# Optimization experiments

Measured on AMD Instinct MI355X. Metric: run time of the kernel, lower is better.

Reference implementation:

```python
import jax, jax.numpy as jnp
from jax import lax
import numpy as np

KSIZE = 3      # matching patch size
RATE = 2       # down/up-sampling rate
STRIDE = 1
FUSE_K = 3     # diagonal fuse kernel (identity eye(3))
SCALE = 10.0   # softmax_scale


def same_pad(H, k, s):
    out = -(-H // s)
    pt = max((out - 1) * s + k - H, 0)
    return (pt // 2, pt - pt // 2)


def extract_patches(x, k, s):
    # x: [C,H,W] -> patches [L, C, k, k] with TF 'SAME' padding (matches torch extract_image_patches)
    C, H, W = x.shape
    ph = same_pad(H, k, s)
    pw = same_pad(W, k, s)
    xp = jnp.pad(x, ((0, 0), ph, pw))
    Hp, Wp = xp.shape[1], xp.shape[2]
    Ho = (Hp - k) // s + 1
    Wo = (Wp - k) // s + 1
    sl = [xp[:, i:i + (Ho - 1) * s + 1:s, j:j + (Wo - 1) * s + 1:s]
          for i in range(k) for j in range(k)]
    p = jnp.stack(sl, axis=1).reshape(C, k, k, Ho * Wo)  # [C,k,k,L]
    return p.transpose(3, 0, 1, 2)  # [L,C,k,k]


def diag_sum(t, k=FUSE_K):
    # conv2d with eye(k) kernel, SAME padding: out[p,q] = sum_d t[p+d-k//2, q+d-k//2]
    p0 = (k - 1) // 2
    p1 = k - 1 - p0
    tp = jnp.pad(t, ((p0, p1), (p0, p1)))
    H, W = t.shape
    return sum(tp[d:d + H, d:d + W] for d in range(k))


def attend_one(fi, bi):
    # fi, bi: [C,H,W] full resolution
    C, H, W = fi.shape
    kernel = 2 * RATE
    # patches for reconstruction, from full-res background
    raw_w = extract_patches(bi, kernel, RATE * STRIDE)  # [L,C,4,4]
    # nearest downsample by rate for matching
    fs = fi[:, ::RATE, ::RATE]
    bs = bi[:, ::RATE, ::RATE]
    Hs, Ws = fs.shape[1], fs.shape[2]
    L = Hs * Ws
    # matching patches from downscaled background, l2-normalized
    w = extract_patches(bs, KSIZE, STRIDE)  # [L,C,3,3]
    norm = jnp.sqrt(jnp.sum(w * w, axis=(1, 2, 3), keepdims=True))
    wn = (w / jnp.maximum(norm, 1e-4)).reshape(L, -1)  # [L, C*9]
    # correlation conv == im2col matmul: yi[l, q] = <patch_l(b), patch_q(f)>
    fp = extract_patches(fs, KSIZE, 1).reshape(L, -1)  # [HWf, C*9]
    yi = jnp.einsum('lp,qp->lq', wn, fp)  # [HWb, HWf]
    # fuse: propagate scores along diagonals in both orderings
    t = diag_sum(yi)
    t = t.reshape(Hs, Ws, Hs, Ws).transpose(1, 0, 3, 2).reshape(L, L)
    t = diag_sum(t)
    yi = t.reshape(Ws, Hs, Ws, Hs).transpose(1, 0, 3, 2).reshape(L, Hs, Ws)
    # softmax over background-patch axis
    att = jax.nn.softmax(yi * SCALE, axis=0)  # [L,Hs,Ws]
    # conv_transpose2d(att, raw_w, stride=2, padding=1) / 4  via overlap-add
    contrib = jnp.einsum('lhw,lcij->cijhw', att, raw_w)  # [C,4,4,Hs,Ws]
    buf = jnp.zeros((C, 2 * Hs + 2, 2 * Ws + 2), fi.dtype)
    for i in range(kernel):
        for j in range(kernel):
            buf = buf.at[:, i:i + 2 * Hs:2, j:j + 2 * Ws:2].add(contrib[:, i, j])
    return buf[:, 1:2 * Hs + 1, 1:2 * Ws + 1] / 4.0  # [C,H,W]


def conv3x3_elu(x, w, bias):
    y = lax.conv_general_dilated(x, w, (1, 1), [(1, 1), (1, 1)],
                                 dimension_numbers=('NCHW', 'OIHW', 'NCHW'))
    return jax.nn.elu(y + bias[None, :, None, None])


def setup_inputs() -> dict:
    key = jax.random.key(0)
    k1, k2, k3, k4 = jax.random.split(key, 4)
    B, C, H, W = 4, 128, 128, 128
    f = jax.random.normal(k1, (B, C, H, W), jnp.float32)
    b = jax.random.normal(k2, (B, C, H, W), jnp.float32)
    w1 = jax.random.normal(k3, (C, C, 3, 3), jnp.float32) * 0.02
    b1 = jnp.zeros((C,), jnp.float32)
    w2 = jax.random.normal(k4, (C, C, 3, 3), jnp.float32) * 0.02
    b2 = jnp.zeros((C,), jnp.float32)
    return {'f': f, 'b': b, 'w1': w1, 'b1': b1, 'w2': w2, 'b2': b2}


def reference(f, b, w1, b1, w2, b2):
    y = jax.vmap(attend_one)(f, b)  # [B,C,H,W]
    y = conv3x3_elu(y, w1, b1)
    y = conv3x3_elu(y, w2, b2)
    return y
```

## Files before the change

### kernel.cpp

```cpp
#include <hip/hip_runtime.h>
#include <math.h>

using u16 = unsigned short;
using u32 = unsigned int;
typedef _Float16 f16x8 __attribute__((ext_vector_type(8)));
typedef float    f32x4 __attribute__((ext_vector_type(4)));

union F16U { _Float16 h; u16 u; };
__device__ __forceinline__ u16 f2h(float f) { F16U x; x.h = (_Float16)f; return x.u; }
__device__ __forceinline__ float h2f(u16 v) { F16U x; x.u = v; return (float)x.h; }

__device__ __forceinline__ void gl16(const void* g, void* l) {
  __builtin_amdgcn_global_load_lds((const __attribute__((address_space(1))) void*)g,
                                   (__attribute__((address_space(3))) void*)l, 16, 0, 0);
}


__global__ void k_wperm(const float* __restrict__ w, u16* __restrict__ Wp) {
  int idx = blockIdx.x * 256 + threadIdx.x;
  if (idx < 147456) {
    int co = idx / 1152, r = idx - co * 1152, tap = r >> 7, ci = r & 127;
    Wp[idx] = f2h(w[((size_t)co * 128 + ci) * 9 + tap]);
  }
}

__global__ void k_extract(const float* __restrict__ fi, const float* __restrict__ bi,
                          u16* __restrict__ fh, u16* __restrict__ fl,
                          u16* __restrict__ bh, u16* __restrict__ bl) {
  __shared__ u16 lt[4][64][136];
  int ph = blockIdx.x, t = threadIdx.x;
  for (int it = 0; it < 32; ++it) {
    int idx = it * 256 + t;
    int c = idx >> 6, pw = idx & 63;
    int src = c * 16384 + (2 * ph) * 128 + 2 * pw;
    float vf = fi[src], vb = bi[src];
    u16 fhi = f2h(vf), flo = f2h(vf - h2f(fhi));
    u16 bhi = f2h(vb), blo = f2h(vb - h2f(bhi));
    lt[0][pw][c] = fhi; lt[1][pw][c] = flo; lt[2][pw][c] = bhi; lt[3][pw][c] = blo;
  }
  __syncthreads();
  for (int it = 0; it < 16; ++it) {
    int g = it * 256 + t;
    int arr = g >> 10, rem = g & 1023, pw = rem >> 4, slot = rem & 15;
    uint4 v = *(const uint4*)&lt[arr][pw][slot * 8];
    u16* o = (arr == 0) ? fh : (arr == 1) ? fl : (arr == 2) ? bh : bl;
    *(uint4*)&o[(size_t)(ph * 64 + pw) * 128 + slot * 8] = v;
  }
}

__global__ void k_norm(const u16* __restrict__ bh, const u16* __restrict__ bl,
                       float* __restrict__ nrm) {
  int wid = threadIdx.x >> 6, lane = threadIdx.x & 63;
  int l = blockIdx.x * 4 + wid;
  int lh = l >> 6, lw = l & 63;
  float s = 0.f;
#pragma unroll
  for (int dh = -1; dh <= 1; ++dh)
#pragma unroll
    for (int dw = -1; dw <= 1; ++dw) {
      int y = lh + dh, x = lw + dw;
      if ((u32)y < 64u && (u32)x < 64u) {
        int p = y * 64 + x;
        u32 h2 = *(const u32*)&bh[(size_t)p * 128 + lane * 2];
        u32 l2 = *(const u32*)&bl[(size_t)p * 128 + lane * 2];
        float v0 = h2f((u16)h2) + h2f((u16)l2);
        float v1 = h2f((u16)(h2 >> 16)) + h2f((u16)(l2 >> 16));
        s += v0 * v0 + v1 * v1;
      }
    }
#pragma unroll
  for (int off = 32; off; off >>= 1) s += __shfl_xor(s, off);
  if (lane == 0) nrm[l] = sqrtf(s);
}

__global__ __launch_bounds__(256) void k_rgemm(const u16* __restrict__ fh, const u16* __restrict__ fl,
                                               const u16* __restrict__ bh, const u16* __restrict__ bl,
                                               float* __restrict__ C) {
  __shared__ u16 lds[4 * 128 * 64];
  u16* Ah = lds; u16* Al = lds + 8192; u16* Bh = lds + 16384; u16* Bl = lds + 24576;
  int t = threadIdx.x, lane = t & 63, wid = t >> 6;
  int wm = (wid >> 1) * 64, wn = (wid & 1) * 64;
  int fr = lane & 15, kb = lane >> 4;
  int b = blockIdx.x;
  int xcd = b & 7, r = b >> 3;
  int by = xcd * 4 + (r & 3), bx = r >> 2;
  int q0 = by * 128, l0 = bx * 128;
  f32x4 acc[4][4] = {};
  for (int kt = 0; kt < 128; kt += 64) {
#pragma unroll
    for (int j = 0; j < 4; ++j) {
      int g = wid * 256 + j * 64 + lane;
      int row = g >> 3, s = (g & 7) ^ (row & 7);
      int co = kt + s * 8;
      size_t ldso = (size_t)(wid * 256 + j * 64) * 8;
      gl16(&fh[(size_t)(q0 + row) * 128 + co], Ah + ldso);
      gl16(&fl[(size_t)(q0 + row) * 128 + co], Al + ldso);
      gl16(&bh[(size_t)(l0 + row) * 128 + co], Bh + ldso);
      gl16(&bl[(size_t)(l0 + row) * 128 + co], Bl + ldso);
    }
    __syncthreads();
#pragma unroll
    for (int kf = 0; kf < 2; ++kf) {
      f16x8 ah[4], al4[4], bh4[4], bl4[4];
#pragma unroll
      for (int mi = 0; mi < 4; ++mi) {
        int row = wm + mi * 16 + fr;
        int off = row * 64 + ((kf * 4 + kb) ^ (row & 7)) * 8;
        ah[mi] = *(const f16x8*)&Ah[off];
        al4[mi] = *(const f16x8*)&Al[off];
      }
#pragma unroll
      for (int ni = 0; ni < 4; ++ni) {
        int row = wn + ni * 16 + fr;
        int off = row * 64 + ((kf * 4 + kb) ^ (row & 7)) * 8;
        bh4[ni] = *(const f16x8*)&Bh[off];
        bl4[ni] = *(const f16x8*)&Bl[off];
      }
#pragma unroll
      for (int mi = 0; mi < 4; ++mi)
#pragma unroll
        for (int ni = 0; ni < 4; ++ni) {
          acc[mi][ni] = __builtin_amdgcn_mfma_f32_16x16x32_f16(ah[mi], bh4[ni], acc[mi][ni], 0, 0, 0);
          acc[mi][ni] = __builtin_amdgcn_mfma_f32_16x16x32_f16(ah[mi], bl4[ni], acc[mi][ni], 0, 0, 0);
          acc[mi][ni] = __builtin_amdgcn_mfma_f32_16x16x32_f16(al4[mi], bh4[ni], acc[mi][ni], 0, 0, 0);
        }
    }
    __syncthreads();
  }
#pragma unroll
  for (int mi = 0; mi < 4; ++mi) {
    int qr = q0 + wm + mi * 16 + kb * 4;
#pragma unroll
    for (int ni = 0; ni < 4; ++ni) {
      int lc = l0 + wn + ni * 16 + fr;
#pragma unroll
      for (int r2 = 0; r2 < 4; ++r2)
        C[(size_t)(qr + r2) * 4096 + lc] = acc[mi][ni][r2];
    }
  }
}

__global__ __launch_bounds__(256) void k_passA(const float* __restrict__ R, const float* __restrict__ nrm,
                                               float* __restrict__ Y0) {
  int b = blockIdx.x;
  int xcd = b & 7, r = b >> 3;
  int q = xcd * 512 + (r >> 2);
  int part = r & 3;
  int l0 = part * 1024 + threadIdx.x * 4;
  int idx0 = q * 4096 + l0;
  int qh = q >> 6, qw = q & 63, lh = l0 >> 6, lw0 = l0 & 63;
  float a0 = 0.f, a1 = 0.f, a2 = 0.f, a3 = 0.f;
#define TAPA(dh, dw)                                                                   \
  {                                                                                    \
    constexpr int s = (dh) * 64 + (dw);                                                \
    constexpr int rr = s & 3;                                                          \
    bool ok = ((u32)(qh + (dh)) < 64u) && ((u32)(qw + (dw)) < 64u) &&                  \
              ((u32)(lh + (dh)) < 64u);                                                \
    int ab = idx0 + s * 4097 - rr;                                                     \
    ab = ab < 0 ? 0 : (ab > 16777208 ? 16777208 : ab);                                 \
    float4 lo = *(const float4*)&R[ab], hi = *(const float4*)&R[ab + 4];               \
    float xx[8] = {lo.x, lo.y, lo.z, lo.w, hi.x, hi.y, hi.z, hi.w};                    \
    if (ok) {                                                                          \
      if ((u32)(lw0 + 0 + (dw)) < 64u) a0 += xx[rr + 0];                               \
      if ((u32)(lw0 + 1 + (dw)) < 64u) a1 += xx[rr + 1];                               \
      if ((u32)(lw0 + 2 + (dw)) < 64u) a2 += xx[rr + 2];                               \
      if ((u32)(lw0 + 3 + (dw)) < 64u) a3 += xx[rr + 3];                               \
    }                                                                                  \
  }
  TAPA(-1, -1) TAPA(-1, 0) TAPA(-1, 1)
  TAPA(0, -1)  TAPA(0, 0)  TAPA(0, 1)
  TAPA(1, -1)  TAPA(1, 0)  TAPA(1, 1)
#undef TAPA
  float4 nv = *(const float4*)&nrm[l0];
  float4 o;
  o.x = a0 / fmaxf(nv.x, 1e-4f);
  o.y = a1 / fmaxf(nv.y, 1e-4f);
  o.z = a2 / fmaxf(nv.z, 1e-4f);
  o.w = a3 / fmaxf(nv.w, 1e-4f);
  *(float4*)&Y0[idx0] = o;
}

__global__ __launch_bounds__(256) void k_pbsm(const float* __restrict__ T1, u16* __restrict__ att) {
  int b = blockIdx.x;
  int q = (b & 7) * 512 + (b >> 3);
  int t = threadIdx.x;
  int qh = q >> 6;
  bool qok = (qh >= 2 && qh <= 61);
  float v[16];
#pragma unroll
  for (int p = 0; p < 4; ++p) {
    int l0 = p * 1024 + t * 4;
    int idx0 = q * 4096 + l0;
    int lh = l0 >> 6;
    float a0 = 0.f, a1 = 0.f, a2 = 0.f, a3 = 0.f;
    if (qok && lh >= 2 && lh <= 61) {
#define TAPB(s_)                                                                       \
  {                                                                                    \
    constexpr int s = (s_);                                                            \
    constexpr int rr = s & 3;                                                          \
    const float* pp = T1 + (idx0 + s * 4097 - rr);                                     \
    float4 lo = *(const float4*)pp, hi = *(const float4*)(pp + 4);                     \
    float xx[8] = {lo.x, lo.y, lo.z, lo.w, hi.x, hi.y, hi.z, hi.w};                    \
    a0 += xx[rr + 0]; a1 += xx[rr + 1]; a2 += xx[rr + 2]; a3 += xx[rr + 3];            \
  }
      TAPB(-65) TAPB(-64) TAPB(-63)
      TAPB(-1)  TAPB(0)   TAPB(1)
      TAPB(63)  TAPB(64)  TAPB(65)
#undef TAPB
    } else {
      float oe[4];
#pragma unroll
      for (int e = 0; e < 4; ++e) {
        int l = l0 + e;
        int pl = ((l & 63) << 6) | (l >> 6);
        int pq = ((q & 63) << 6) | (q >> 6);
        float acc = 0.f;
#pragma unroll
        for (int e2 = -1; e2 <= 1; ++e2) {
          int pa = pl + e2, pb = pq + e2;
          if ((u32)pa < 4096u && (u32)pb < 4096u) {
            int a = ((pa & 63) << 6) | (pa >> 6);
            int bq = ((pb & 63) << 6) | (pb >> 6);
#pragma unroll
            for (int e1 = -1; e1 <= 1; ++e1) {
              int aa = a + e1, bb = bq + e1;
              if ((u32)aa < 4096u && (u32)bb < 4096u) acc += T1[(size_t)bb * 4096 + aa];
            }
          }
        }
        oe[e] = acc;
      }
      a0 = oe[0]; a1 = oe[1]; a2 = oe[2]; a3 = oe[3];
    }
    v[p * 4 + 0] = a0; v[p * 4 + 1] = a1; v[p * 4 + 2] = a2; v[p * 4 + 3] = a3;
  }
  float m = -3.4e38f;
#pragma unroll
  for (int i = 0; i < 16; ++i) m = fmaxf(m, v[i]);
#pragma unroll
  for (int off = 32; off; off >>= 1) m = fmaxf(m, __shfl_xor(m, off));
  __shared__ float redm[4], reds[4];
  int wid = t >> 6, lane = t & 63;
  if (lane == 0) redm[wid] = m;
  __syncthreads();
  m = fmaxf(fmaxf(redm[0], redm[1]), fmaxf(redm[2], redm[3]));
  float s = 0.f;
#pragma unroll
  for (int i = 0; i < 16; ++i) { v[i] = expf(10.f * (v[i] - m)); s += v[i]; }
#pragma unroll
  for (int off = 32; off; off >>= 1) s += __shfl_xor(s, off);
  if (lane == 0) reds[wid] = s;
  __syncthreads();
  s = reds[0] + reds[1] + reds[2] + reds[3];
  float inv = 1.f / s;
  u16* arow = att + (size_t)q * 4096;
#pragma unroll
  for (int p = 0; p < 4; ++p) {
    union { u16 h[4]; uint2 u; } pk;
    pk.h[0] = f2h(v[p * 4 + 0] * inv); pk.h[1] = f2h(v[p * 4 + 1] * inv);
    pk.h[2] = f2h(v[p * 4 + 2] * inv); pk.h[3] = f2h(v[p * 4 + 3] * inv);
    *(uint2*)&arow[p * 1024 + t * 4] = pk.u;
  }
}

__global__ void k_rwt(const float* __restrict__ bi, u16* __restrict__ RWt) {
  int tid = blockIdx.x * 256 + threadIdx.x;
  int m = tid >> 10, lq = (tid & 1023) * 4;
  int c = m >> 4, i = (m >> 2) & 3, j = m & 3;
  int y = 2 * (lq >> 6) - 1 + i;
  union { u16 h[4]; uint2 u; } pk;
#pragma unroll
  for (int e = 0; e < 4; ++e) {
    int x = 2 * ((lq + e) & 63) - 1 + j;
    float v = 0.f;
    if ((u32)y < 128u && (u32)x < 128u) v = bi[c * 16384 + y * 128 + x];
    pk.h[e] = f2h(v);
  }
  *(uint2*)&RWt[(size_t)m * 4096 + lq] = pk.u;
}

__global__ __launch_bounds__(256) void k_gemm_pv(const u16* __restrict__ A, const u16* __restrict__ Bt,
                                                 float* __restrict__ C) {
  __shared__ u16 lds[2 * 16384];
  int t = threadIdx.x, lane = t & 63, wid = t >> 6;
  int wm = (wid >> 1) * 64, wn = (wid & 1) * 64;
  int fr = lane & 15, kb = lane >> 4;
  int bid = blockIdx.x;
  int my = (bid & 7) * 4 + ((bid >> 3) & 3);
  int nx = bid >> 5;
  int m0 = my * 128, n0 = nx * 128;
  f32x4 acc[4][4] = {};
#define STAGE(buf, kt)                                                                  \
  {                                                                                     \
    u16* lA = lds + (buf) * 16384;                                                      \
    u16* lB = lA + 8192;                                                                \
    _Pragma("unroll")                                                                   \
    for (int j = 0; j < 4; ++j) {                                                       \
      int g = wid * 256 + j * 64 + lane;                                                \
      int row = g >> 3, sw = (g & 7) ^ (row & 7);                                       \
      size_t ldso = (size_t)(wid * 256 + j * 64) * 8;                                   \
      gl16(&A[(size_t)(m0 + row) * 4096 + (kt) + sw * 8], lA + ldso);                   \
      gl16(&Bt[(size_t)(n0 + row) * 4096 + (kt) + sw * 8], lB + ldso);                  \
    }                                                                                   \
  }
  STAGE(0, 0)
  __syncthreads();
  int cur = 0;
  for (int kt = 0; kt < 4096; kt += 64) {
    if (kt + 64 < 4096) STAGE(cur ^ 1, kt + 64)
    u16* la = lds + cur * 16384;
    u16* lb = la + 8192;
#pragma unroll
    for (int ks = 0; ks < 2; ++ks) {
      f16x8 af[4], bfr[4];
#pragma unroll
      for (int mi = 0; mi < 4; ++mi) {
        int row = wm + mi * 16 + fr;
        af[mi] = *(const f16x8*)&la[row * 64 + ((ks * 32 + kb * 8) ^ ((row & 7) << 3))];
      }
#pragma unroll
      for (int ni = 0; ni < 4; ++ni) {
        int row = wn + ni * 16 + fr;
        bfr[ni] = *(const f16x8*)&lb[row * 64 + ((ks * 32 + kb * 8) ^ ((row & 7) << 3))];
      }
#pragma unroll
      for (int mi = 0; mi < 4; ++mi)
#pragma unroll
        for (int ni = 0; ni < 4; ++ni)
          acc[mi][ni] = __builtin_amdgcn_mfma_f32_16x16x32_f16(af[mi], bfr[ni], acc[mi][ni], 0, 0, 0);
    }
    __syncthreads();
    cur ^= 1;
  }
#undef STAGE
#pragma unroll
  for (int mi = 0; mi < 4; ++mi) {
    int mr = m0 + wm + mi * 16 + kb * 4;
#pragma unroll
    for (int ni = 0; ni < 4; ++ni) {
      int nc = n0 + wn + ni * 16 + fr;
#pragma unroll
      for (int r = 0; r < 4; ++r)
        C[(size_t)(mr + r) * 2048 + nc] = acc[mi][ni][r];
    }
  }
}

__global__ void k_overlap(const float* __restrict__ O, u16* __restrict__ Yh) {
  int b = blockIdx.x;
  int xcd = b & 7, r = b >> 3;
  int oypair = xcd * 8 + (r & 7);
  int c = r >> 3;
  int t = threadIdx.x;
  int idx = c * 16384 + oypair * 256 + t;
  int ox = idx & 127, oy = (idx & 16383) >> 7;
  int py = oy + 1, px = ox + 1;
  float s = 0.f;
#pragma unroll
  for (int di = 0; di < 2; ++di) {
    int i = (py & 1) + 2 * di;
    int hs = (py - i) >> 1;
    if ((u32)hs >= 64u) continue;
#pragma unroll
    for (int dj = 0; dj < 2; ++dj) {
      int j = (px & 1) + 2 * dj;
      int wsx = (px - j) >> 1;
      if ((u32)wsx >= 64u) continue;
      s += O[(size_t)(hs * 64 + wsx) * 2048 + c * 16 + i * 4 + j];
    }
  }
  Yh[((size_t)oy * 128 + ox) * 128 + c] = f2h(0.25f * s);
}

template<int OUT_F16>
__global__ __launch_bounds__(256) void k_conv(const u16* __restrict__ In, const u16* __restrict__ Wp,
                                              const float* __restrict__ bias, void* __restrict__ out_,
                                              const u16* __restrict__ zg) {
  __shared__ u16 lds[2 * 128 * 64];
  u16* la = lds; u16* lb = lds + 8192;
  int t = threadIdx.x, lane = t & 63, wid = t >> 6;
  int wm = (wid >> 1) * 64, wn = (wid & 1) * 64;
  int fr = lane & 15, kb = lane >> 4;
  int yrow = blockIdx.x, bidx = blockIdx.y;
  const u16* inH = In + (size_t)bidx * 2097152;
  f32x4 acc[4][4] = {};
  for (int step = 0; step < 18; ++step) {
    int tap = step >> 1, ci0 = (step & 1) * 64;
    int dy = tap / 3, dx = tap - 3 * (tap / 3);
    int y = yrow + dy - 1;
#pragma unroll
    for (int j = 0; j < 4; ++j) {
      int g = wid * 256 + j * 64 + lane;
      int row = g >> 3, s = (g & 7) ^ (row & 7);
      size_t ldso = (size_t)(wid * 256 + j * 64) * 8;
      gl16(&Wp[(size_t)row * 1152 + step * 64 + s * 8], la + ldso);
      int xx = row + dx - 1;
      const u16* src = ((u32)y < 128u && (u32)xx < 128u)
                         ? &inH[((size_t)y * 128 + xx) * 128 + ci0 + s * 8] : zg;
      gl16(src, lb + ldso);
    }
    __syncthreads();
#pragma unroll
    for (int ks = 0; ks < 2; ++ks) {
      f16x8 af[4], bfr[4];
#pragma unroll
      for (int mi = 0; mi < 4; ++mi) {
        int row = wm + mi * 16 + fr;
        af[mi] = *(const f16x8*)&la[row * 64 + ((ks * 32 + kb * 8) ^ ((row & 7) << 3))];
      }
#pragma unroll
      for (int ni = 0; ni < 4; ++ni) {
        int row = wn + ni * 16 + fr;
        bfr[ni] = *(const f16x8*)&lb[row * 64 + ((ks * 32 + kb * 8) ^ ((row & 7) << 3))];
      }
#pragma unroll
      for (int mi = 0; mi < 4; ++mi)
#pragma unroll
        for (int ni = 0; ni < 4; ++ni)
          acc[mi][ni] = __builtin_amdgcn_mfma_f32_16x16x32_f16(af[mi], bfr[ni], acc[mi][ni], 0, 0, 0);
    }
    __syncthreads();
  }
#pragma unroll
  for (int mi = 0; mi < 4; ++mi) {
    int co = wm + mi * 16 + kb * 4;
#pragma unroll
    for (int ni = 0; ni < 4; ++ni) {
      int x = wn + ni * 16 + fr;
      if (OUT_F16) {
        union { u16 h[4]; uint2 v; } pk;
#pragma unroll
        for (int r = 0; r < 4; ++r) {
          float val = acc[mi][ni][r] + bias[co + r];
          val = val > 0.f ? val : expm1f(val);
          pk.h[r] = f2h(val);
        }
        u16* oH = (u16*)out_ + (size_t)bidx * 2097152;
        *(uint2*)&oH[((size_t)yrow * 128 + x) * 128 + co] = pk.v;
      } else {
        float* oF = (float*)out_ + (size_t)bidx * 2097152;
#pragma unroll
        for (int r = 0; r < 4; ++r) {
          float val = acc[mi][ni][r] + bias[co + r];
          val = val > 0.f ? val : expm1f(val);
          oF[(size_t)(co + r) * 16384 + yrow * 128 + x] = val;
        }
      }
    }
  }
}


extern "C" void kernel_launch(void* const* d_in, const int* in_sizes, int n_in,
                              void* d_out, int out_size, void* d_ws, size_t ws_size,
                              hipStream_t stream) {
  const float* f  = (const float*)d_in[0];
  const float* b  = (const float*)d_in[1];
  const float* w1 = (const float*)d_in[2];
  const float* b1 = (const float*)d_in[3];
  const float* w2 = (const float*)d_in[4];
  const float* b2 = (const float*)d_in[5];
  float* out = (float*)d_out;
  char* ws = (char*)d_ws;

  float* S0   = (float*)(ws);
  float* S1   = (float*)(ws + 67108864);
  u16*   fsTh = (u16*)(ws + 134217728);
  u16*   fsTl = (u16*)(ws + 135266304);
  u16*   bsTh = (u16*)(ws + 136314880);
  u16*   bsTl = (u16*)(ws + 137363456);
  float* nrm  = (float*)(ws + 138412032);
  u16*   Yh   = (u16*)(ws + 138428416);
  u16*   Wp1  = (u16*)(ws + 155205632);
  u16*   Wp2  = (u16*)(ws + 155500544);
  u16*   att  = (u16*)S0;
  u16*   RWt  = (u16*)S1;
  float* O    = (float*)(ws + 67108864 + 16777216);
  u16*   Z1h  = (u16*)S0;
  u16*   zg   = (u16*)(ws + 50331648);

  k_wperm<<<576, 256, 0, stream>>>(w1, Wp1);
  k_wperm<<<576, 256, 0, stream>>>(w2, Wp2);

  for (int i = 0; i < 4; ++i) {
    const float* fb = f + (size_t)i * 2097152;
    const float* bb = b + (size_t)i * 2097152;
    k_extract<<<64, 256, 0, stream>>>(fb, bb, fsTh, fsTl, bsTh, bsTl);
    k_norm<<<1024, 256, 0, stream>>>(bsTh, bsTl, nrm);
    k_rgemm<<<1024, 256, 0, stream>>>(fsTh, fsTl, bsTh, bsTl, S0);
    k_passA<<<16384, 256, 0, stream>>>(S0, nrm, S1);
    k_pbsm<<<4096, 256, 0, stream>>>(S1, att);
    k_rwt<<<8192, 256, 0, stream>>>(bb, RWt);
    k_gemm_pv<<<512, 256, 0, stream>>>(att, RWt, O);
    k_overlap<<<8192, 256, 0, stream>>>(O, Yh + (size_t)i * 2097152);
  }

  hipMemsetAsync(zg, 0, 256, stream);
  k_conv<1><<<dim3(128, 4), 256, 0, stream>>>(Yh, Wp1, b1, Z1h, zg);
  k_conv<0><<<dim3(128, 4), 256, 0, stream>>>(Z1h, Wp2, b2, out, zg);

  (void)in_sizes; (void)n_in; (void)out_size; (void)ws_size;
}
```

Before: 1.072 ms.

## Store correlation scores in diagonal-major layout to make diag-sum passes contiguous

The correlation GEMM now stages its tile in LDS and writes results in a diagonal-indexed layout (row = (q-l) mod 4096), so both diagonal-fuse passes read contiguous neighbours instead of strided 4097-offset gathers. The second fuse pass writes scores back to row-major through an LDS transpose, and softmax moves into its own kernel. This adds an extra full-matrix write/read pass and an extra launch in exchange for coalesced diagonal access, and it reshuffles the workspace buffers.

```diff
diff --git a/kernel.cpp b/kernel.cpp
--- a/kernel.cpp
+++ b/kernel.cpp
@@ -127,116 +127,152 @@
     }
     __syncthreads();
   }
+  float* TC = (float*)lds;
 #pragma unroll
   for (int mi = 0; mi < 4; ++mi) {
-    int qr = q0 + wm + mi * 16 + kb * 4;
+    int qr = wm + mi * 16 + kb * 4;
 #pragma unroll
     for (int ni = 0; ni < 4; ++ni) {
-      int lc = l0 + wn + ni * 16 + fr;
+      int lc = wn + ni * 16 + fr;
 #pragma unroll
       for (int r2 = 0; r2 < 4; ++r2)
-        C[(size_t)(qr + r2) * 4096 + lc] = acc[mi][ni][r2];
-    }
-  }
-}
-
-__global__ __launch_bounds__(256) void k_passA(const float* __restrict__ R, const float* __restrict__ nrm,
-                                               float* __restrict__ Y0) {
+        TC[(qr + r2) * 128 + lc] = acc[mi][ni][r2];
+    }
+  }
+  __syncthreads();
+  int dq0l0 = q0 - l0;
+  for (int dd = wid * 64; dd < wid * 64 + 64; ++dd) {
+    if (dd >= 255) break;
+    int d = dd - 127;
+    int jst = d < 0 ? -d : 0;
+    int len = 128 - (d < 0 ? -d : d);
+    int drow = (dq0l0 + d) & 4095;
+#pragma unroll
+    for (int ro = 0; ro < 2; ++ro) {
+      int j = jst + ro * 64 + lane;
+      if (j < jst + len)
+        C[(size_t)drow * 4096 + l0 + j] = TC[(j + d) * 128 + j];
+    }
+  }
+}
+
+__global__ __launch_bounds__(256) void k_passA(const float* __restrict__ Rd, const float* __restrict__ nrm,
+                                               float* __restrict__ Yd) {
+  int tid = blockIdx.x * 256 + threadIdx.x;
+  int drow = tid >> 9;
+  int u0 = (tid & 511) * 8;
+  float buf[3][16];
+#pragma unroll
+  for (int c = 0; c < 3; ++c) {
+    int base = drow * 4096 + u0 + (c - 1) * 64 - 4;
+#pragma unroll
+    for (int kk = 0; kk < 4; ++kk) {
+      int a = base + kk * 4;
+      a = a < 0 ? 0 : (a > 16777212 ? 16777212 : a);
+      *(float4*)&buf[c][kk * 4] = *(const float4*)&Rd[a];
+    }
+  }
+  float4 nv0 = *(const float4*)&nrm[u0];
+  float4 nv1 = *(const float4*)&nrm[u0 + 4];
+  float nvv[8] = {nv0.x, nv0.y, nv0.z, nv0.w, nv1.x, nv1.y, nv1.z, nv1.w};
+  float out[8];
+#pragma unroll
+  for (int e = 0; e < 8; ++e) {
+    int l = u0 + e;
+    int q = (drow + l) & 4095;
+    int lh = l >> 6, lw = l & 63, qh = q >> 6, qw = q & 63;
+    float a = 0.f;
+#pragma unroll
+    for (int c = 0; c < 3; ++c) {
+      bool mh = ((u32)(qh + c - 1) < 64u) && ((u32)(lh + c - 1) < 64u);
+#pragma unroll
+      for (int d = 0; d < 3; ++d) {
+        bool mw = ((u32)(qw + d - 1) < 64u) && ((u32)(lw + d - 1) < 64u);
+        if (mh && mw) a += buf[c][e + d + 3];
+      }
+    }
+    out[e] = a / fmaxf(nvv[e], 1e-4f);
+  }
+  *(float4*)&Yd[(size_t)drow * 4096 + u0] = make_float4(out[0], out[1], out[2], out[3]);
+  *(float4*)&Yd[(size_t)drow * 4096 + u0 + 4] = make_float4(out[4], out[5], out[6], out[7]);
+}
+
+__global__ __launch_bounds__(256) void k_pbsm(const float* __restrict__ Yd, float* __restrict__ S) {
+  __shared__ float ST[64][65];
   int b = blockIdx.x;
-  int xcd = b & 7, r = b >> 3;
-  int q = xcd * 512 + (r >> 2);
-  int part = r & 3;
-  int l0 = part * 1024 + threadIdx.x * 4;
-  int idx0 = q * 4096 + l0;
-  int qh = q >> 6, qw = q & 63, lh = l0 >> 6, lw0 = l0 & 63;
-  float a0 = 0.f, a1 = 0.f, a2 = 0.f, a3 = 0.f;
-#define TAPA(dh, dw)                                                                   \
-  {                                                                                    \
-    constexpr int s = (dh) * 64 + (dw);                                                \
-    constexpr int rr = s & 3;                                                          \
-    bool ok = ((u32)(qh + (dh)) < 64u) && ((u32)(qw + (dw)) < 64u) &&                  \
-              ((u32)(lh + (dh)) < 64u);                                                \
-    int ab = idx0 + s * 4097 - rr;                                                     \
-    ab = ab < 0 ? 0 : (ab > 16777208 ? 16777208 : ab);                                 \
-    float4 lo = *(const float4*)&R[ab], hi = *(const float4*)&R[ab + 4];               \
-    float xx[8] = {lo.x, lo.y, lo.z, lo.w, hi.x, hi.y, hi.z, hi.w};                    \
-    if (ok) {                                                                          \
-      if ((u32)(lw0 + 0 + (dw)) < 64u) a0 += xx[rr + 0];                               \
-      if ((u32)(lw0 + 1 + (dw)) < 64u) a1 += xx[rr + 1];                               \
-      if ((u32)(lw0 + 2 + (dw)) < 64u) a2 += xx[rr + 2];                               \
-      if ((u32)(lw0 + 3 + (dw)) < 64u) a3 += xx[rr + 3];                               \
-    }                                                                                  \
-  }
-  TAPA(-1, -1) TAPA(-1, 0) TAPA(-1, 1)
-  TAPA(0, -1)  TAPA(0, 0)  TAPA(0, 1)
-  TAPA(1, -1)  TAPA(1, 0)  TAPA(1, 1)
-#undef TAPA
-  float4 nv = *(const float4*)&nrm[l0];
-  float4 o;
-  o.x = a0 / fmaxf(nv.x, 1e-4f);
-  o.y = a1 / fmaxf(nv.y, 1e-4f);
-  o.z = a2 / fmaxf(nv.z, 1e-4f);
-  o.w = a3 / fmaxf(nv.w, 1e-4f);
-  *(float4*)&Y0[idx0] = o;
-}
-
-__global__ __launch_bounds__(256) void k_pbsm(const float* __restrict__ T1, u16* __restrict__ att) {
-  int b = blockIdx.x;
-  int q = (b & 7) * 512 + (b >> 3);
+  int d0 = (b >> 6) * 64, u0 = (b & 63) * 64;
   int t = threadIdx.x;
-  int qh = q >> 6;
-  bool qok = (qh >= 2 && qh <= 61);
-  float v[16];
-#pragma unroll
-  for (int p = 0; p < 4; ++p) {
-    int l0 = p * 1024 + t * 4;
-    int idx0 = q * 4096 + l0;
-    int lh = l0 >> 6;
-    float a0 = 0.f, a1 = 0.f, a2 = 0.f, a3 = 0.f;
-    if (qok && lh >= 2 && lh <= 61) {
-#define TAPB(s_)                                                                       \
-  {                                                                                    \
-    constexpr int s = (s_);                                                            \
-    constexpr int rr = s & 3;                                                          \
-    const float* pp = T1 + (idx0 + s * 4097 - rr);                                     \
-    float4 lo = *(const float4*)pp, hi = *(const float4*)(pp + 4);                     \
-    float xx[8] = {lo.x, lo.y, lo.z, lo.w, hi.x, hi.y, hi.z, hi.w};                    \
-    a0 += xx[rr + 0]; a1 += xx[rr + 1]; a2 += xx[rr + 2]; a3 += xx[rr + 3];            \
-  }
-      TAPB(-65) TAPB(-64) TAPB(-63)
-      TAPB(-1)  TAPB(0)   TAPB(1)
-      TAPB(63)  TAPB(64)  TAPB(65)
-#undef TAPB
+  int dl = t >> 2, us = (t & 3) * 16;
+  int drow = d0 + dl;
+  int ub = u0 + us;
+  int lh = u0 >> 6;
+  bool lhok = (lh >= 2 && lh <= 61);
+  float buf[3][24];
+  if (lhok) {
+#pragma unroll
+    for (int c = 0; c < 3; ++c) {
+      int base = drow * 4096 + ub + (c - 1) * 64 - 4;
+#pragma unroll
+      for (int kk = 0; kk < 6; ++kk)
+        *(float4*)&buf[c][kk * 4] = *(const float4*)&Yd[base + kk * 4];
+    }
+  }
+#pragma unroll
+  for (int e = 0; e < 16; ++e) {
+    int l = ub + e;
+    int q = (drow + l) & 4095;
+    int qh = q >> 6;
+    float a;
+    if (lhok && qh >= 2 && qh <= 61) {
+      a = 0.f;
+#pragma unroll
+      for (int c = 0; c < 3; ++c)
+#pragma unroll
+        for (int d = 0; d < 3; ++d) a += buf[c][e + d + 3];
     } else {
-      float oe[4];
-#pragma unroll
-      for (int e = 0; e < 4; ++e) {
-        int l = l0 + e;
-        int pl = ((l & 63) << 6) | (l >> 6);
-        int pq = ((q & 63) << 6) | (q >> 6);
-        float acc = 0.f;
-#pragma unroll
-        for (int e2 = -1; e2 <= 1; ++e2) {
-          int pa = pl + e2, pb = pq + e2;
-          if ((u32)pa < 4096u && (u32)pb < 4096u) {
-            int a = ((pa & 63) << 6) | (pa >> 6);
-            int bq = ((pb & 63) << 6) | (pb >> 6);
-#pragma unroll
-            for (int e1 = -1; e1 <= 1; ++e1) {
-              int aa = a + e1, bb = bq + e1;
-              if ((u32)aa < 4096u && (u32)bb < 4096u) acc += T1[(size_t)bb * 4096 + aa];
-            }
+      int pl = ((l & 63) << 6) | (l >> 6);
+      int pq = ((q & 63) << 6) | (q >> 6);
+      a = 0.f;
+      for (int e2 = -1; e2 <= 1; ++e2) {
+        int pa = pl + e2, pb = pq + e2;
+        if ((u32)pa < 4096u && (u32)pb < 4096u) {
+          int aa0 = ((pa & 63) << 6) | (pa >> 6);
+          int bb0 = ((pb & 63) << 6) | (pb >> 6);
+          for (int e1 = -1; e1 <= 1; ++e1) {
+            int aa = aa0 + e1, bb = bb0 + e1;
+            if ((u32)aa < 4096u && (u32)bb < 4096u)
+              a += Yd[(size_t)((bb - aa) & 4095) * 4096 + aa];
           }
         }
-        oe[e] = acc;
-      }
-      a0 = oe[0]; a1 = oe[1]; a2 = oe[2]; a3 = oe[3];
-    }
-    v[p * 4 + 0] = a0; v[p * 4 + 1] = a1; v[p * 4 + 2] = a2; v[p * 4 + 3] = a3;
-  }
+      }
+    }
+    ST[dl][us + e] = a;
+  }
+  __syncthreads();
+  int w = t >> 6, lane = t & 63;
+  for (int jj = 0; jj < 32; ++jj) {
+    int j = w * 32 + jj;
+    if (j >= 127) break;
+    int jm = j < 63 ? j : 63;
+    int dd = jm - lane;
+    int ul = j - dd;
+    if (dd >= 0 && ul < 64) {
+      int q = (d0 + u0 + j) & 4095;
+      S[(size_t)q * 4096 + u0 + ul] = ST[dd][ul];
+    }
+  }
+}
+
+__global__ __launch_bounds__(256) void k_softmax(const float* __restrict__ S, u16* __restrict__ att) {
+  int q = blockIdx.x, t = threadIdx.x;
+  const float* row = S + (size_t)q * 4096;
+  float4 v[4];
   float m = -3.4e38f;
 #pragma unroll
-  for (int i = 0; i < 16; ++i) m = fmaxf(m, v[i]);
+  for (int i = 0; i < 4; ++i) {
+    v[i] = *(const float4*)&row[i * 1024 + t * 4];
+    m = fmaxf(m, fmaxf(fmaxf(v[i].x, v[i].y), fmaxf(v[i].z, v[i].w)));
+  }
 #pragma unroll
   for (int off = 32; off; off >>= 1) m = fmaxf(m, __shfl_xor(m, off));
   __shared__ float redm[4], reds[4];
@@ -246,7 +282,11 @@
   m = fmaxf(fmaxf(redm[0], redm[1]), fmaxf(redm[2], redm[3]));
   float s = 0.f;
 #pragma unroll
-  for (int i = 0; i < 16; ++i) { v[i] = expf(10.f * (v[i] - m)); s += v[i]; }
+  for (int i = 0; i < 4; ++i) {
+    v[i].x = expf(10.f * (v[i].x - m)); v[i].y = expf(10.f * (v[i].y - m));
+    v[i].z = expf(10.f * (v[i].z - m)); v[i].w = expf(10.f * (v[i].w - m));
+    s += v[i].x + v[i].y + v[i].z + v[i].w;
+  }
 #pragma unroll
   for (int off = 32; off; off >>= 1) s += __shfl_xor(s, off);
   if (lane == 0) reds[wid] = s;
@@ -255,11 +295,11 @@
   float inv = 1.f / s;
   u16* arow = att + (size_t)q * 4096;
 #pragma unroll
-  for (int p = 0; p < 4; ++p) {
+  for (int i = 0; i < 4; ++i) {
     union { u16 h[4]; uint2 u; } pk;
-    pk.h[0] = f2h(v[p * 4 + 0] * inv); pk.h[1] = f2h(v[p * 4 + 1] * inv);
-    pk.h[2] = f2h(v[p * 4 + 2] * inv); pk.h[3] = f2h(v[p * 4 + 3] * inv);
-    *(uint2*)&arow[p * 1024 + t * 4] = pk.u;
+    pk.h[0] = f2h(v[i].x * inv); pk.h[1] = f2h(v[i].y * inv);
+    pk.h[2] = f2h(v[i].z * inv); pk.h[3] = f2h(v[i].w * inv);
+    *(uint2*)&arow[i * 1024 + t * 4] = pk.u;
   }
 }
 
@@ -473,9 +513,12 @@
   u16*   Yh   = (u16*)(ws + 138428416);
   u16*   Wp1  = (u16*)(ws + 155205632);
   u16*   Wp2  = (u16*)(ws + 155500544);
-  u16*   att  = (u16*)S0;
-  u16*   RWt  = (u16*)S1;
-  float* O    = (float*)(ws + 67108864 + 16777216);
+  float* Rd   = S0;
+  float* Yd   = S1;
+  float* Ssc  = S0;
+  u16*   att  = (u16*)S1;
+  u16*   RWt  = (u16*)(ws + 67108864 + 33554432);
+  float* O    = S0;
   u16*   Z1h  = (u16*)S0;
   u16*   zg   = (u16*)(ws + 50331648);
 
@@ -487,9 +530,10 @@
     const float* bb = b + (size_t)i * 2097152;
     k_extract<<<64, 256, 0, stream>>>(fb, bb, fsTh, fsTl, bsTh, bsTl);
     k_norm<<<1024, 256, 0, stream>>>(bsTh, bsTl, nrm);
-    k_rgemm<<<1024, 256, 0, stream>>>(fsTh, fsTl, bsTh, bsTl, S0);
-    k_passA<<<16384, 256, 0, stream>>>(S0, nrm, S1);
-    k_pbsm<<<4096, 256, 0, stream>>>(S1, att);
+    k_rgemm<<<1024, 256, 0, stream>>>(fsTh, fsTl, bsTh, bsTl, Rd);
+    k_passA<<<8192, 256, 0, stream>>>(Rd, nrm, Yd);
+    k_pbsm<<<4096, 256, 0, stream>>>(Yd, Ssc);
+    k_softmax<<<4096, 256, 0, stream>>>(Ssc, att);
     k_rwt<<<8192, 256, 0, stream>>>(bb, RWt);
     k_gemm_pv<<<512, 256, 0, stream>>>(att, RWt, O);
     k_overlap<<<8192, 256, 0, stream>>>(O, Yh + (size_t)i * 2097152);
```

Result: slower. 1.838 ms (+71.5%).
